# Optimization experiments

Measured on AMD Instinct MI355X. Metric: run time of the kernel, lower is better.

Reference implementation:

```python
import jax, jax.numpy as jnp
import numpy as np
import math

M = 0.2
S = 30.0
COS_M = math.cos(M)
SIN_M = math.sin(M)
TH = math.cos(math.pi - M)
MM = math.sin(math.pi - M) * M


def setup_inputs() -> dict:
    key = jax.random.key(0)
    k1, k2, k3 = jax.random.split(key, 3)
    B, D, C = 1024, 192, 100000
    x = jax.random.normal(k1, (B, D), dtype=jnp.float32)
    weight = jax.random.normal(k2, (C, D), dtype=jnp.float32)
    label = jax.random.randint(k3, (B,), 0, C, dtype=jnp.int64)
    return {"x": x, "weight": weight, "label": label}


def _l2norm(v, axis=-1, eps=1e-12):
    # matches F.normalize(p=2): v / max(||v||, eps)
    n = jnp.sqrt(jnp.sum(v * v, axis=axis, keepdims=True))
    return v / jnp.maximum(n, eps)


def reference(x, weight, label):
    B = x.shape[0]
    cosine = _l2norm(x) @ _l2norm(weight).T            # [B, C]
    sine = jnp.sqrt(jnp.clip(1.0 - cosine * cosine, 0.0, 1.0))
    phi = cosine * COS_M - sine * SIN_M
    phi = jnp.where(cosine - TH > 0, phi, cosine - MM)
    one_hot = jax.nn.one_hot(label, cosine.shape[1], dtype=cosine.dtype)
    output = (one_hot * phi + (1.0 - one_hot) * cosine) * S
    # cross entropy (mean reduction)
    logp = jax.nn.log_softmax(output, axis=-1)
    loss = -jnp.mean(jnp.take_along_axis(logp, label[:, None], axis=1)[:, 0])
    # top-1 accuracy (percent), detached metric
    pred = jnp.argmax(output, axis=-1)
    prec1 = jnp.mean((pred == label).astype(jnp.float32)) * 100.0
    return loss, prec1
```

## Files before the change

### kernel.cpp

```cpp
#include <hip/hip_runtime.h>
#include <math.h>

#define B_ROWS   1024
#define DIM      192
#define NCLS     100000
#define S_SCALE  30.0f
#define COS_M    0.98006657784124163f
#define SIN_M    0.19866933079506122f
#define TH_C     (-0.98006657784124163f)
#define MM_C     0.039733866159012243f
#define L2E30    43.2808512266689f
#define EXPM30   9.357622968840175e-14f
#define LN2_C    0.69314718055994531f

#define NTILE_B  784
#define NCHUNKR  16
#define ASEG_CH  1536
#define NSLOT    1568

#define NCHUNKC  1568
#define CSPLIT   128
#define NSLOT2   128
#define PACK_WGRID 3136
#define PACK_GRID  3168

typedef float floatx4 __attribute__((ext_vector_type(4)));
typedef __bf16 bf16x8 __attribute__((ext_vector_type(8)));

#define AS1 __attribute__((address_space(1)))
#define AS3 __attribute__((address_space(3)))

__device__ __forceinline__ unsigned int f2bf(float x) {
    unsigned int u = __float_as_uint(x);
    u = (u + 0x7fffu + ((u >> 16) & 1u)) >> 16;
    return u;
}
__device__ __forceinline__ unsigned int pack2(float lo, float hi) {
    return f2bf(lo) | (f2bf(hi) << 16);
}
__device__ __forceinline__ float fexp2(float x) {
#if __has_builtin(__builtin_amdgcn_exp2f)
    return __builtin_amdgcn_exp2f(x);
#else
    float r; __asm__("v_exp_f32 %0, %1" : "=v"(r) : "v"(x)); return r;
#endif
}
template <int N>
__device__ __forceinline__ float ror16(float x) {
    return __int_as_float(__builtin_amdgcn_mov_dpp(
        __float_as_int(x), 0x120 | N, 0xF, 0xF, false));
}
__device__ __forceinline__ void gload_lds16(const void* g, void* l) {
    __builtin_amdgcn_global_load_lds(
        (const AS1 unsigned int*)g, (AS3 unsigned int*)l, 16, 0, 0);
}
__device__ __forceinline__ void waitcnt_vm(int pend) {
    if (pend >= 2)      asm volatile("s_waitcnt vmcnt(12)" ::: "memory");
    else if (pend == 1) asm volatile("s_waitcnt vmcnt(6)"  ::: "memory");
    else                asm volatile("s_waitcnt vmcnt(0)"  ::: "memory");
    __builtin_amdgcn_sched_barrier(0);
}


__global__ __launch_bounds__(256)
void pack2_kernel(const float* __restrict__ x, const float* __restrict__ w,
                  unsigned short* __restrict__ asw, unsigned short* __restrict__ wsw,
                  float* __restrict__ accum)
{
    __shared__ uint4 lds_pk[32][25];
    const int bid = blockIdx.x;
    const int t = threadIdx.x;
    const int r = t >> 3, oct = t & 7;

    const float* src;
    unsigned short* dstc;
    int rowbase, half;
    bool wside;
    if (bid < PACK_WGRID) {
        const int k = bid & 7, j = bid >> 3;
        int cs, cc, h;
        if (j < 104) {
            const int i = j / 26; h = j % 26;
            cs = k + 8 * i;  cc = cs * 13 + (h >> 1);
        } else {
            const int j2 = j - 104;
            const int i = 4 + j2 / 24; h = j2 % 24;
            cs = k + 8 * i;  cc = 416 + (cs - 32) * 12 + (h >> 1);
        }
        half = h & 1;
        rowbase = cc * 64 + half * 32;
        src = w;  dstc = wsw + (size_t)cc * 12288;  wside = true;
    } else {
        const int xb = bid - PACK_WGRID;
        half = xb & 1;
        rowbase = xb * 32;
        src = x;  dstc = asw + (size_t)(xb >> 1) * 12288;  wside = false;
        if (bid == PACK_WGRID && t < 4) accum[t] = 0.0f;
    }

    const int row = rowbase + r;
    const bool live = !wside || (row < NCLS);
    float4 buf[6];
    float s = 0.f;
    if (live) {
        const float4* sp = (const float4*)(src + (size_t)row * DIM) + oct * 6;
        #pragma unroll
        for (int q = 0; q < 6; ++q) {
            float4 v = sp[q];
            buf[q] = v;
            s += v.x * v.x + v.y * v.y + v.z * v.z + v.w * v.w;
        }
    } else {
        #pragma unroll
        for (int q = 0; q < 6; ++q) buf[q] = make_float4(0.f, 0.f, 0.f, 0.f);
    }
    s += __shfl_xor(s, 1);
    s += __shfl_xor(s, 2);
    s += __shfl_xor(s, 4);
    float inv = live ? (1.0f / fmaxf(sqrtf(s), 1e-12f)) : 0.0f;
    if (!wside) inv *= L2E30;

    #pragma unroll
    for (int j = 0; j < 3; ++j) {
        const int k8 = oct * 3 + j;
        uint4 o;
        float4 a0 = buf[2 * j], a1 = buf[2 * j + 1];
        o.x = pack2(a0.x * inv, a0.y * inv);
        o.y = pack2(a0.z * inv, a0.w * inv);
        o.z = pack2(a1.x * inv, a1.y * inv);
        o.w = pack2(a1.z * inv, a1.w * inv);
        lds_pk[r][k8] = o;
    }
    __syncthreads();
    #pragma unroll
    for (int j = 0; j < 3; ++j) {
        const int flat = j * 256 + t;
        const int sseg = flat >> 5, rr = flat & 31;
        *(uint4*)(dstc + ((size_t)(sseg * 64) + half * 32 + rr) * 8)
            = lds_pk[rr][sseg];
    }
}

__global__ __launch_bounds__(256, 2)
void gemm_stats10_kernel(const unsigned short* __restrict__ asw,
                         const unsigned short* __restrict__ wsw,
                         float2* __restrict__ pslot)
{
    __shared__ __align__(16) char lds[73728];
    const int bid  = blockIdx.x;
    const int cs   = bid & 127;
    const int rb   = bid >> 7;
    const int tid  = threadIdx.x;
    const int wv   = tid >> 6;
    const int lane = tid & 63;
    const int quad = lane >> 4, mrow = lane & 15;

    bf16x8 xfr[4][6];
    {
        const unsigned short* ab = asw + (size_t)(rb * 4 + wv) * 12288;
        #pragma unroll
        for (int a = 0; a < 4; ++a)
            #pragma unroll
            for (int ks = 0; ks < 6; ++ks)
                xfr[a][ks] = *(const bf16x8*)(ab +
                    (size_t)((ks * 4 + quad) * 64 + a * 16 + mrow) * 8);
    }

    const int nch = 12 + (cs < 32 ? 1 : 0);
    const char* wp0 = (const char*)(wsw
                    + (size_t)(cs * 12 + (cs < 32 ? cs : 32)) * 12288);
    const int soff = wv * 6144 + lane * 16;
    const int loff = wv * 6144;

    float s_acc[4][4];
    float m_acc[4][4];
    #pragma unroll
    for (int a = 0; a < 4; ++a)
        #pragma unroll
        for (int r = 0; r < 4; ++r) { s_acc[a][r] = 0.f; m_acc[a][r] = -1e30f; }

    {
        const char* g0 = wp0 + soff;
        #pragma unroll
        for (int i = 0; i < 6; ++i)
            gload_lds16(g0 + i * 1024, lds + loff + i * 1024);
        const char* g1 = wp0 + 24576 + soff;
        #pragma unroll
        for (int i = 0; i < 6; ++i)
            gload_lds16(g1 + i * 1024, lds + 24576 + loff + i * 1024);
    }

    #pragma unroll 1
    for (int c = 0; c < nch; ++c) {
        if (c + 2 < nch) {
            const char* g = wp0 + (size_t)(c + 2) * 24576 + soff;
            char* l = lds + ((c + 2) % 3) * 24576 + loff;
            #pragma unroll
            for (int i = 0; i < 6; ++i)
                gload_lds16(g + i * 1024, l + i * 1024);
        }
        int pend = nch - 1 - c; if (pend > 2) pend = 2;
        waitcnt_vm(pend);
        __builtin_amdgcn_s_barrier();

        const char* bb = lds + (c % 3) * 24576;
        floatx4 acc[4][4];
        #pragma unroll
        for (int a = 0; a < 4; ++a)
            #pragma unroll
            for (int ni = 0; ni < 4; ++ni) {
                floatx4 z = {0.f, 0.f, 0.f, 0.f};
                acc[a][ni] = z;
            }
        #pragma unroll
        for (int ks = 0; ks < 6; ++ks) {
            const char* sb = bb + (size_t)((ks * 4 + quad) * 64 + mrow) * 16;
            bf16x8 b0 = *(const bf16x8*)(sb);
            bf16x8 b1 = *(const bf16x8*)(sb + 256);
            bf16x8 b2 = *(const bf16x8*)(sb + 512);
            bf16x8 b3 = *(const bf16x8*)(sb + 768);
            __builtin_amdgcn_s_setprio(1);
            #pragma unroll
            for (int a = 0; a < 4; ++a) {
                acc[a][0] = __builtin_amdgcn_mfma_f32_16x16x32_bf16(
                    xfr[a][ks], b0, acc[a][0], 0, 0, 0);
                acc[a][1] = __builtin_amdgcn_mfma_f32_16x16x32_bf16(
                    xfr[a][ks], b1, acc[a][1], 0, 0, 0);
                acc[a][2] = __builtin_amdgcn_mfma_f32_16x16x32_bf16(
                    xfr[a][ks], b2, acc[a][2], 0, 0, 0);
                acc[a][3] = __builtin_amdgcn_mfma_f32_16x16x32_bf16(
                    xfr[a][ks], b3, acc[a][3], 0, 0, 0);
            }
            __builtin_amdgcn_s_setprio(0);
        }
        #pragma unroll
        for (int a = 0; a < 4; ++a)
            #pragma unroll
            for (int r = 0; r < 4; ++r) {
                float v0 = acc[a][0][r], v1 = acc[a][1][r];
                float v2 = acc[a][2][r], v3 = acc[a][3][r];
                m_acc[a][r] = fmaxf(fmaxf(fmaxf(fmaxf(v0, v1), v2), v3),
                                    m_acc[a][r]);
                s_acc[a][r] += (fexp2(v0) + fexp2(v1))
                             + (fexp2(v2) + fexp2(v3));
            }
        __builtin_amdgcn_s_barrier();
    }

    const int rowb = rb * 256 + wv * 64;
    #pragma unroll
    for (int a = 0; a < 4; ++a)
        #pragma unroll
        for (int r = 0; r < 4; ++r) {
            float s = s_acc[a][r], m = m_acc[a][r];
            s += ror16<1>(s); s += ror16<2>(s); s += ror16<4>(s); s += ror16<8>(s);
            m = fmaxf(m, ror16<1>(m)); m = fmaxf(m, ror16<2>(m));
            m = fmaxf(m, ror16<4>(m)); m = fmaxf(m, ror16<8>(m));
            if (mrow == 0)
                pslot[(size_t)cs * B_ROWS + rowb + a * 16 + quad * 4 + r] =
                    make_float2(m, s);
        }
}

__global__ __launch_bounds__(256)
void finalize2_kernel(const float2* __restrict__ pslot,
                      const float* __restrict__ x, const float* __restrict__ w,
                      const int* __restrict__ label,
                      float* __restrict__ accum, float* __restrict__ out)
{
    __shared__ float2 red[8][32];
    const int t = threadIdx.x, rr = t & 31, g = t >> 5;
    {
        const int row = blockIdx.x * 32 + rr;
        float M = -1e30f, L = 0.f;
        #pragma unroll
        for (int s = 0; s < NSLOT2 / 8; ++s) {
            float2 p = pslot[(size_t)(s * 8 + g) * B_ROWS + row];
            M = fmaxf(M, p.x);
            L += p.y;
        }
        red[g][rr] = make_float2(M, L);
    }
    __syncthreads();
    if (t < 32) {
        const int row = blockIdx.x * 32 + t;
        float Mc = -1e30f, L = 0.f;
        #pragma unroll
        for (int g2 = 0; g2 < 8; ++g2) {
            float2 p = red[g2][t];
            Mc = fmaxf(Mc, p.x);
            L += p.y;
        }

        const int lab = label[row];
        const float4* xr = (const float4*)(x + (size_t)row * DIM);
        const float4* wr = (const float4*)(w + (size_t)lab * DIM);
        float dot = 0.f, nx = 0.f, nw = 0.f;
        #pragma unroll
        for (int q = 0; q < 48; ++q) {
            float4 a = xr[q], b = wr[q];
            dot += a.x * b.x + a.y * b.y + a.z * b.z + a.w * b.w;
            nx  += a.x * a.x + a.y * a.y + a.z * a.z + a.w * a.w;
            nw  += b.x * b.x + b.y * b.y + b.z * b.z + b.w * b.w;
        }
        float cosl    = dot / fmaxf(sqrtf(nx) * sqrtf(nw), 1e-12f);
        float t_plain = S_SCALE * cosl;
        float sine    = sqrtf(fmaxf(0.f, fminf(1.f, 1.f - cosl * cosl)));
        float phi     = cosl * COS_M - sine * SIN_M;
        float modv    = ((cosl - TH_C) > 0.f) ? phi : (cosl - MM_C);
        float t_mod   = S_SCALE * modv;

        float Ladj = L * EXPM30 - __expf(t_plain - 30.0f) + __expf(t_mod - 30.0f);
        Ladj = fmaxf(Ladj, 1e-37f);
        float loss = (30.0f + logf(Ladj)) - t_mod;
        float corr = (t_mod > Mc * LN2_C) ? 1.f : 0.f;

        #pragma unroll
        for (int off = 16; off > 0; off >>= 1) {
            loss += __shfl_xor(loss, off);
            corr += __shfl_xor(corr, off);
        }
        if (t == 0) {
            atomicAdd(&accum[0], loss);
            atomicAdd(&accum[1], corr);
            __threadfence();
            int old = atomicAdd((int*)accum + 2, 1);
            if (old == (int)gridDim.x - 1) {
                float a0 = atomicAdd(&accum[0], 0.0f);
                float a1 = atomicAdd(&accum[1], 0.0f);
                out[0] = a0 * (1.0f / (float)B_ROWS);
                out[1] = a1 * (100.0f / (float)B_ROWS);
            }
        }
    }
}


__global__ __launch_bounds__(256)
void prep_kernel(const float* __restrict__ x, unsigned short* __restrict__ asw,
                 float* __restrict__ accum)
{
    const int ab = blockIdx.x;
    const int t = threadIdx.x;
    if (ab == 0 && t < 4) accum[t] = 0.0f;
    const int r = t >> 1, half = t & 1;
    const int row = ab * 128 + r;
    const int c = ab * 2 + (r >> 6);
    const int r64 = r & 63;

    float4 buf[24];
    float s = 0.f;
    const float4* sp = (const float4*)(x + (size_t)row * DIM) + half * 24;
    #pragma unroll
    for (int q = 0; q < 24; ++q) {
        float4 v = sp[q];
        buf[q] = v;
        s += v.x * v.x + v.y * v.y + v.z * v.z + v.w * v.w;
    }
    s += __shfl_xor(s, 1);
    const float inv = 1.0f / fmaxf(sqrtf(s), 1e-12f);
    #pragma unroll
    for (int j = 0; j < 12; ++j) {
        const int k8 = half * 12 + j;
        uint4 o;
        float4 a0 = buf[2 * j], a1 = buf[2 * j + 1];
        o.x = pack2(a0.x * inv, a0.y * inv);
        o.y = pack2(a0.z * inv, a0.w * inv);
        o.z = pack2(a1.x * inv, a1.y * inv);
        o.w = pack2(a1.z * inv, a1.w * inv);
        *(uint4*)(asw + ((size_t)c * ASEG_CH + k8 * 64 + r64) * 8) = o;
    }
}

__global__ __launch_bounds__(256, 3)
void gemm_stats_kernel(const float* __restrict__ w,
                       const unsigned short* __restrict__ asw,
                       unsigned int* __restrict__ pslot)
{
    __shared__ __align__(16) char lds[49152];
    const int tid  = threadIdx.x;
    const int wave = tid >> 6;
    const int lane = tid & 63;
    const int quad = lane >> 4;
    const int mrow = lane & 15;
    const int rg   = wave >> 1;
    const int cgr  = wave & 1;

    {
        const int r = tid >> 1, half = tid & 1;
        const int col = blockIdx.x * 128 + r;
        const bool live = (col < NCLS);
        float4 buf[24];
        float s = 0.f;
        if (live) {
            const float4* sp = (const float4*)(w + (size_t)col * DIM) + half * 24;
            #pragma unroll
            for (int q = 0; q < 24; ++q) {
                float4 v = sp[q];
                buf[q] = v;
                s += v.x * v.x + v.y * v.y + v.z * v.z + v.w * v.w;
            }
        }
        s += __shfl_xor(s, 1);
        const float inv = live ? (1.0f / fmaxf(sqrtf(s), 1e-12f)) : 0.0f;
        #pragma unroll
        for (int j = 0; j < 12; ++j) {
            const int k8 = half * 12 + j;
            uint4 o = make_uint4(0u, 0u, 0u, 0u);
            if (live) {
                float4 a0 = buf[2 * j], a1 = buf[2 * j + 1];
                o.x = pack2(a0.x * inv, a0.y * inv);
                o.y = pack2(a0.z * inv, a0.w * inv);
                o.z = pack2(a1.x * inv, a1.y * inv);
                o.w = pack2(a1.z * inv, a1.w * inv);
            }
            *(uint4*)(lds + (size_t)(k8 * 128 + r) * 16) = o;
        }
    }
    __syncthreads();

    bf16x8 bfr[6][4];
    #pragma unroll
    for (int ks = 0; ks < 6; ++ks)
        #pragma unroll
        for (int ni = 0; ni < 4; ++ni)
            bfr[ks][ni] = *(const bf16x8*)(lds +
                (((ks * 4 + quad) * 128) + cgr * 64 + ni * 16 + mrow) * 16);

    const int slot = blockIdx.x * 2 + cgr;
    #pragma unroll 2
    for (int c = 0; c < NCHUNKR; ++c) {
        const unsigned short* ab = asw + (size_t)c * ASEG_CH * 8;
        floatx4 acc[2][4];
        #pragma unroll
        for (int mi = 0; mi < 2; ++mi)
            #pragma unroll
            for (int ni = 0; ni < 4; ++ni) {
                floatx4 z = {0.f, 0.f, 0.f, 0.f};
                acc[mi][ni] = z;
            }
        #pragma unroll
        for (int ks = 0; ks < 6; ++ks) {
            bf16x8 a0 = *(const bf16x8*)(ab +
                (size_t)(((ks * 4 + quad) * 64) + rg * 32 + mrow) * 8);
            bf16x8 a1 = *(const bf16x8*)(ab +
                (size_t)(((ks * 4 + quad) * 64) + rg * 32 + 16 + mrow) * 8);
            #pragma unroll
            for (int ni = 0; ni < 4; ++ni)
                acc[0][ni] = __builtin_amdgcn_mfma_f32_16x16x32_bf16(
                    a0, bfr[ks][ni], acc[0][ni], 0, 0, 0);
            #pragma unroll
            for (int ni = 0; ni < 4; ++ni)
                acc[1][ni] = __builtin_amdgcn_mfma_f32_16x16x32_bf16(
                    a1, bfr[ks][ni], acc[1][ni], 0, 0, 0);
        }

        #pragma unroll
        for (int mi = 0; mi < 2; ++mi)
            #pragma unroll
            for (int r = 0; r < 4; ++r) {
                float v0 = acc[mi][0][r], v1 = acc[mi][1][r];
                float v2 = acc[mi][2][r], v3 = acc[mi][3][r];
                float m = fmaxf(fmaxf(v0, v1), fmaxf(v2, v3));
                float s = fexp2(fmaf(v0, L2E30, -L2E30))
                        + fexp2(fmaf(v1, L2E30, -L2E30))
                        + fexp2(fmaf(v2, L2E30, -L2E30))
                        + fexp2(fmaf(v3, L2E30, -L2E30));
                s += ror16<1>(s); s += ror16<2>(s);
                s += ror16<4>(s); s += ror16<8>(s);
                m = fmaxf(m, ror16<1>(m)); m = fmaxf(m, ror16<2>(m));
                m = fmaxf(m, ror16<4>(m)); m = fmaxf(m, ror16<8>(m));
                if (mrow == mi * 4 + r)
                    pslot[(size_t)slot * B_ROWS +
                          c * 64 + rg * 32 + mi * 16 + quad * 4 + r] = pack2(m, s);
            }
    }
}

__global__ __launch_bounds__(256)
void finalize_kernel(const unsigned int* __restrict__ pslot,
                     const float* __restrict__ x, const float* __restrict__ w,
                     const int* __restrict__ label,
                     float* __restrict__ accum, float* __restrict__ out)
{
    __shared__ float2 red[8][32];
    const int t = threadIdx.x, rr = t & 31, g = t >> 5;
    {
        const int row = blockIdx.x * 32 + rr;
        float M = -1e30f, L = 0.f;
        for (int s = g; s < NSLOT; s += 8) {
            unsigned int u = pslot[(size_t)s * B_ROWS + row];
            M = fmaxf(M, __uint_as_float(u << 16));
            L += __uint_as_float(u & 0xFFFF0000u);
        }
        red[g][rr] = make_float2(M, L);
    }
    __syncthreads();
    if (t < 32) {
        const int row = blockIdx.x * 32 + t;
        float Mc = -1e30f, L = 0.f;
        #pragma unroll
        for (int g2 = 0; g2 < 8; ++g2) {
            float2 p = red[g2][t];
            Mc = fmaxf(Mc, p.x);
            L += p.y;
        }

        const int lab = label[row];
        const float4* xr = (const float4*)(x + (size_t)row * DIM);
        const float4* wr = (const float4*)(w + (size_t)lab * DIM);
        float dot = 0.f, nx = 0.f, nw = 0.f;
        #pragma unroll
        for (int q = 0; q < 48; ++q) {
            float4 a = xr[q], b = wr[q];
            dot += a.x * b.x + a.y * b.y + a.z * b.z + a.w * b.w;
            nx  += a.x * a.x + a.y * a.y + a.z * a.z + a.w * a.w;
            nw  += b.x * b.x + b.y * b.y + b.z * b.z + b.w * b.w;
        }
        float cosl    = dot / fmaxf(sqrtf(nx) * sqrtf(nw), 1e-12f);
        float t_plain = S_SCALE * cosl;
        float sine    = sqrtf(fmaxf(0.f, fminf(1.f, 1.f - cosl * cosl)));
        float phi     = cosl * COS_M - sine * SIN_M;
        float modv    = ((cosl - TH_C) > 0.f) ? phi : (cosl - MM_C);
        float t_mod   = S_SCALE * modv;

        float Ladj = L - __expf(t_plain - 30.0f) + __expf(t_mod - 30.0f);
        Ladj = fmaxf(Ladj, 1e-37f);
        float loss = (30.0f + logf(Ladj)) - t_mod;
        float corr = (t_mod > S_SCALE * Mc) ? 1.f : 0.f;

        #pragma unroll
        for (int off = 16; off > 0; off >>= 1) {
            loss += __shfl_xor(loss, off);
            corr += __shfl_xor(corr, off);
        }
        if (t == 0) {
            atomicAdd(&accum[0], loss);
            atomicAdd(&accum[1], corr);
            __threadfence();
            int old = atomicAdd((int*)accum + 2, 1);
            if (old == (int)gridDim.x - 1) {
                float a0 = atomicAdd(&accum[0], 0.0f);
                float a1 = atomicAdd(&accum[1], 0.0f);
                out[0] = a0 * (1.0f / (float)B_ROWS);
                out[1] = a1 * (100.0f / (float)B_ROWS);
            }
        }
    }
}

extern "C" void kernel_launch(void* const* d_in, const int* in_sizes, int n_in,
                              void* d_out, int out_size, void* d_ws, size_t ws_size,
                              hipStream_t stream)
{
    const float* x     = (const float*)d_in[0];
    const float* w     = (const float*)d_in[1];
    const int*   label = (const int*)d_in[2];
    float* out = (float*)d_out;

    char* ws = (char*)d_ws;
    float* accum = (float*)ws;
    unsigned short* asw = (unsigned short*)(ws + 256);
    const size_t asw_bytes = (size_t)NCHUNKR * ASEG_CH * 16;

    const size_t wsw_bytes    = (size_t)NCHUNKC * 24 * 64 * 16;
    const size_t pslot2_bytes = (size_t)NSLOT2 * B_ROWS * 8;
    const size_t need_new = 256 + asw_bytes + wsw_bytes + pslot2_bytes;

    if (ws_size >= need_new) {
        unsigned short* wsw = (unsigned short*)(ws + 256 + asw_bytes);
        float2* pslot2 = (float2*)(ws + 256 + asw_bytes + wsw_bytes);
        pack2_kernel<<<dim3(PACK_GRID), dim3(256), 0, stream>>>(x, w, asw, wsw, accum);
        gemm_stats10_kernel<<<dim3(4 * CSPLIT), dim3(256), 0, stream>>>(asw, wsw, pslot2);
        finalize2_kernel<<<dim3(B_ROWS / 32), dim3(256), 0, stream>>>(
            pslot2, x, w, label, accum, out);
    } else {
        unsigned int* pslot = (unsigned int*)(ws + 256 + asw_bytes);
        prep_kernel<<<dim3(8), dim3(256), 0, stream>>>(x, asw, accum);
        gemm_stats_kernel<<<dim3(NTILE_B), dim3(256), 0, stream>>>(w, asw, pslot);
        finalize_kernel<<<dim3(B_ROWS / 32), dim3(256), 0, stream>>>(
            pslot, x, w, label, accum, out);
    }
}
```

Before: 159.3 us.

## Software-pipeline MFMA halves with exp/max epilogue in GEMM stats kernel

Splits each chunk's 4 column-tile MFMA accumulators into two halves (A and B). The exp2/max/sum epilogue of one half is interleaved with the MFMAs of the other half, with the B half's epilogue deferred into the next chunk. The aim is to hide transcendental and VALU epilogue latency behind matrix-core work instead of running them serially. The cost is more live accumulator registers across iterations, plus an extra tail epilogue after the loop.

```diff
diff --git a/kernel.cpp b/kernel.cpp
--- a/kernel.cpp
+++ b/kernel.cpp
@@ -142,7 +142,7 @@
 }
 
 __global__ __launch_bounds__(256, 2)
-void gemm_stats10_kernel(const unsigned short* __restrict__ asw,
+void gemm_stats12_kernel(const unsigned short* __restrict__ asw,
                          const unsigned short* __restrict__ wsw,
                          float2* __restrict__ pslot)
 {
@@ -190,6 +190,8 @@
             gload_lds16(g1 + i * 1024, lds + 24576 + loff + i * 1024);
     }
 
+    floatx4 accB[4][2];
+
     #pragma unroll 1
     for (int c = 0; c < nch; ++c) {
         if (c + 2 < nch) {
@@ -204,48 +206,82 @@
         __builtin_amdgcn_s_barrier();
 
         const char* bb = lds + (c % 3) * 24576;
-        floatx4 acc[4][4];
+
+        floatx4 accA[4][2];
         #pragma unroll
         for (int a = 0; a < 4; ++a)
             #pragma unroll
-            for (int ni = 0; ni < 4; ++ni) {
+            for (int p = 0; p < 2; ++p) {
                 floatx4 z = {0.f, 0.f, 0.f, 0.f};
-                acc[a][ni] = z;
+                accA[a][p] = z;
             }
         #pragma unroll
         for (int ks = 0; ks < 6; ++ks) {
             const char* sb = bb + (size_t)((ks * 4 + quad) * 64 + mrow) * 16;
             bf16x8 b0 = *(const bf16x8*)(sb);
             bf16x8 b1 = *(const bf16x8*)(sb + 256);
+            __builtin_amdgcn_s_setprio(1);
+            #pragma unroll
+            for (int a = 0; a < 4; ++a) {
+                accA[a][0] = __builtin_amdgcn_mfma_f32_16x16x32_bf16(
+                    xfr[a][ks], b0, accA[a][0], 0, 0, 0);
+                accA[a][1] = __builtin_amdgcn_mfma_f32_16x16x32_bf16(
+                    xfr[a][ks], b1, accA[a][1], 0, 0, 0);
+            }
+            __builtin_amdgcn_s_setprio(0);
+            if (ks < 4 && c > 0) {
+                const int a = ks;
+                #pragma unroll
+                for (int r = 0; r < 4; ++r) {
+                    float v0 = accB[a][0][r], v1 = accB[a][1][r];
+                    m_acc[a][r] = fmaxf(fmaxf(v0, v1), m_acc[a][r]);
+                    s_acc[a][r] += fexp2(v0) + fexp2(v1);
+                }
+            }
+        }
+
+        #pragma unroll
+        for (int a = 0; a < 4; ++a)
+            #pragma unroll
+            for (int p = 0; p < 2; ++p) {
+                floatx4 z = {0.f, 0.f, 0.f, 0.f};
+                accB[a][p] = z;
+            }
+        #pragma unroll
+        for (int ks = 0; ks < 6; ++ks) {
+            const char* sb = bb + (size_t)((ks * 4 + quad) * 64 + mrow) * 16;
             bf16x8 b2 = *(const bf16x8*)(sb + 512);
             bf16x8 b3 = *(const bf16x8*)(sb + 768);
             __builtin_amdgcn_s_setprio(1);
             #pragma unroll
             for (int a = 0; a < 4; ++a) {
-                acc[a][0] = __builtin_amdgcn_mfma_f32_16x16x32_bf16(
-                    xfr[a][ks], b0, acc[a][0], 0, 0, 0);
-                acc[a][1] = __builtin_amdgcn_mfma_f32_16x16x32_bf16(
-                    xfr[a][ks], b1, acc[a][1], 0, 0, 0);
-                acc[a][2] = __builtin_amdgcn_mfma_f32_16x16x32_bf16(
-                    xfr[a][ks], b2, acc[a][2], 0, 0, 0);
-                acc[a][3] = __builtin_amdgcn_mfma_f32_16x16x32_bf16(
-                    xfr[a][ks], b3, acc[a][3], 0, 0, 0);
+                accB[a][0] = __builtin_amdgcn_mfma_f32_16x16x32_bf16(
+                    xfr[a][ks], b2, accB[a][0], 0, 0, 0);
+                accB[a][1] = __builtin_amdgcn_mfma_f32_16x16x32_bf16(
+                    xfr[a][ks], b3, accB[a][1], 0, 0, 0);
             }
             __builtin_amdgcn_s_setprio(0);
-        }
-        #pragma unroll
-        for (int a = 0; a < 4; ++a)
-            #pragma unroll
-            for (int r = 0; r < 4; ++r) {
-                float v0 = acc[a][0][r], v1 = acc[a][1][r];
-                float v2 = acc[a][2][r], v3 = acc[a][3][r];
-                m_acc[a][r] = fmaxf(fmaxf(fmaxf(fmaxf(v0, v1), v2), v3),
-                                    m_acc[a][r]);
-                s_acc[a][r] += (fexp2(v0) + fexp2(v1))
-                             + (fexp2(v2) + fexp2(v3));
-            }
+            if (ks < 4) {
+                const int a = ks;
+                #pragma unroll
+                for (int r = 0; r < 4; ++r) {
+                    float v0 = accA[a][0][r], v1 = accA[a][1][r];
+                    m_acc[a][r] = fmaxf(fmaxf(v0, v1), m_acc[a][r]);
+                    s_acc[a][r] += fexp2(v0) + fexp2(v1);
+                }
+            }
+        }
         __builtin_amdgcn_s_barrier();
     }
+
+    #pragma unroll
+    for (int a = 0; a < 4; ++a)
+        #pragma unroll
+        for (int r = 0; r < 4; ++r) {
+            float v0 = accB[a][0][r], v1 = accB[a][1][r];
+            m_acc[a][r] = fmaxf(fmaxf(v0, v1), m_acc[a][r]);
+            s_acc[a][r] += fexp2(v0) + fexp2(v1);
+        }
 
     const int rowb = rb * 256 + wv * 64;
     #pragma unroll
@@ -571,7 +607,7 @@
         unsigned short* wsw = (unsigned short*)(ws + 256 + asw_bytes);
         float2* pslot2 = (float2*)(ws + 256 + asw_bytes + wsw_bytes);
         pack2_kernel<<<dim3(PACK_GRID), dim3(256), 0, stream>>>(x, w, asw, wsw, accum);
-        gemm_stats10_kernel<<<dim3(4 * CSPLIT), dim3(256), 0, stream>>>(asw, wsw, pslot2);
+        gemm_stats12_kernel<<<dim3(4 * CSPLIT), dim3(256), 0, stream>>>(asw, wsw, pslot2);
         finalize2_kernel<<<dim3(B_ROWS / 32), dim3(256), 0, stream>>>(
             pslot2, x, w, label, accum, out);
     } else {
```

New measurement: 161.0 us. No clear change (+1.0%).
